# Kernel optimization log

Hardware: AMD Instinct MI355X
Metric: run time of the kernel (lower is better)

The kernel has to match this reference:

```python
import jax, jax.numpy as jnp
import numpy as np

N_SAMPLES = 32768


def fft_shift(a, shift):
    n = a.shape[-1]
    shift_samples = shift * (n / 3.0)  # trailing dim of shift is 1 -> broadcasts over coeffs
    pad = [(0, 0)] * (a.ndim - 1) + [(0, 2 * n)]
    spec = jnp.fft.rfft(jnp.pad(a, pad), axis=-1, norm='ortho')
    n_coeffs = spec.shape[-1]
    phase = jnp.arange(n_coeffs) * (2j * jnp.pi / n_coeffs)
    spec = spec * jnp.exp(-phase * shift_samples)
    out = jnp.fft.irfft(spec, n=3 * n, axis=-1, norm='ortho')
    return out[..., :n]


def interp_linear(x, out_size):
    # matches torch F.interpolate(mode='linear', align_corners=False)
    in_size = x.shape[-1]
    scale = in_size / out_size
    coords = (jnp.arange(out_size, dtype=x.dtype) + 0.5) * scale - 0.5
    coords = jnp.clip(coords, 0.0, in_size - 1)
    i0 = jnp.floor(coords).astype(jnp.int32)
    i1 = jnp.minimum(i0 + 1, in_size - 1)
    w = coords - i0.astype(x.dtype)
    return x[..., i0] * (1.0 - w) + x[..., i1] * w


def instrument(t, shift, energy, properties):
    batch, n_events, time_len = t.shape
    t = fft_shift(t, shift)  # (b,e,T)
    _, _, cp, n_frames = energy.shape
    frame_shifts = jnp.linspace(0.0, 1.0, n_frames)
    # (b,e,1,T) shifted per-frame -> (b,e,F,T)
    exp_t = fft_shift(t[:, :, None, :], frame_shifts[None, None, :, None])
    exp_t = exp_t[:, :, None, :, :]  # (b,e,1,F,T)
    # triu mask with offset 2: mask[i,j]=1 iff j >= i+2
    mask = (jnp.arange(time_len)[None, :] >= (jnp.arange(n_frames)[:, None] + 2)).astype(t.dtype)
    mask = fft_shift(mask[None, None], shift[:, :, None, :])  # (b,e,F,T)
    mass = properties[..., :1, None]      # (b,e,cp,1,1)
    friction = properties[..., 1:, None]  # (b,e,cp,1,1)
    x = energy[..., None] * jnp.exp(-friction / (2.0 * mass) * exp_t)  # (b,e,cp,F,T)
    x = x * mask[:, :, None, :, :]
    return jnp.sum(x, axis=-2)  # (b,e,cp,T)


def reference(time, shifts, energy, shape, properties, w_pos, b_pos, w_layers, b_layers):
    batch, n_events, cp, n_frames = energy.shape
    channels, enc = w_pos.shape
    # positional filterbank -> embed -> (1,1,channels,N)
    freqs = jnp.linspace(1e-05, 0.5, enc)
    tt = jnp.linspace(0.0, float(N_SAMPLES), N_SAMPLES)
    p = jnp.sin(tt[:, None] * freqs[None, :] * jnp.pi)  # (N, enc)
    pos = (p @ w_pos.T + b_pos).T[None, None]  # (1,1,channels,N)
    # envelopes
    env = instrument(time, shifts, energy, properties)  # (b,e,cp,T)
    env = jax.nn.relu(interp_linear(env, N_SAMPLES))    # (b,e,cp,N)
    # shape network (residual layers use only l2: x + l2(relu(x)))
    s = jnp.swapaxes(shape, -1, -2)  # (b,e,F,channels)
    for i in range(w_layers.shape[0]):
        s = s + jax.nn.relu(s) @ w_layers[i].T + b_layers[i]
    s = jax.nn.relu(s)
    s = jnp.swapaxes(s, -1, -2)           # (b,e,channels,F)
    s = interp_linear(s, N_SAMPLES)       # (b,e,channels,N)
    x = pos * s * env                      # cp == channels
    return jnp.sum(x, axis=2)              # (b,e,N)


def setup_inputs():
    key = jax.random.key(0)
    ks = jax.random.split(key, 9)
    B, E, CP, F_, T, CH, ENC, L = 2, 8, 32, 64, 2048, 32, 256, 4
    return {
        'time': jax.random.uniform(ks[0], (B, E, T), dtype=jnp.float32),
        'shifts': jax.random.uniform(ks[1], (B, E, 1), dtype=jnp.float32),
        'energy': jax.random.uniform(ks[2], (B, E, CP, F_), dtype=jnp.float32),
        'shape': jax.random.normal(ks[3], (B, E, CH, F_), dtype=jnp.float32),
        'properties': jax.random.uniform(ks[4], (B, E, CP, 2), dtype=jnp.float32) + 0.5,
        'w_pos': jax.random.normal(ks[5], (CH, ENC), dtype=jnp.float32) * 0.06,
        'b_pos': jax.random.normal(ks[6], (CH,), dtype=jnp.float32) * 0.02,
        'w_layers': jax.random.normal(ks[7], (L, CH, CH), dtype=jnp.float32) * 0.15,
        'b_layers': jax.random.normal(ks[8], (L, CH), dtype=jnp.float32) * 0.02,
    }
```

## Files before the change

### kernel.cpp

```cpp
#include <hip/hip_runtime.h>
#include <math.h>

#define TL 2048
#define PI_D 3.14159265358979323846

typedef __attribute__((ext_vector_type(8))) short short8v;
typedef __attribute__((ext_vector_type(4))) float float4v;

#define REPLEN 392
#define REPB (REPLEN * 2)
#define OFF_B 8192

__device__ __forceinline__ unsigned short bf16_rne(float f) {
  unsigned u = __float_as_uint(f);
  return (unsigned short)((u + 0x7FFFu + ((u >> 16) & 1u)) >> 16);
}

__device__ __forceinline__ float tap_val(int idx, double beta, double wv) {
  int d = idx - 2047;
  double x = PI_D * (double)d / 6144.0 - beta;
  if (fabs(x) < 1e-9) return 1.0f;
  double c = wv * (cos(x) / sin(x));
  if (d & 1) c = -c;
  return (float)c;
}

__global__ __launch_bounds__(256) void build_shift_k(const float* __restrict__ shifts,
                                                     const float* __restrict__ time_in,
                                                     float* __restrict__ kerC,
                                                     unsigned short* __restrict__ BFrep,
                                                     unsigned short* __restrict__ tsh_b) {
  __shared__ __align__(16) unsigned char sm1[17408];
  __shared__ float wsum[4];
  int b = blockIdx.x;
  int tid = threadIdx.x;
  if (b < 80) {
    float* kf = (float*)sm1;
    double s;
    if (b < 64) s = (double)b * (1.0 / 63.0) * (2048.0 / 3.0);
    else        s = (double)shifts[b - 64] * (2048.0 / 3.0);
    double beta = PI_D * s / 3073.0;
    double y = 3072.0 * s / 3073.0;
    double r = y - rint(y);
    double wv = -sin(2.0 * PI_D * r) / 6144.0;
    for (int idx = tid; idx < 4104; idx += 256)
      kf[idx] = (idx < 4095) ? tap_val(idx, beta, wv) : 0.0f;
    __syncthreads();
    if (b < 64) {
      for (int c = tid; c < 4096; c += 256) {
        int sr = c >> 9;
        int m = c & 511;
        int A = 4095 - 8 * m + sr;
        unsigned short out[8];
#pragma unroll
        for (int rr = 0; rr < 8; ++rr) out[rr] = bf16_rne(kf[A - rr]);
        *(short8v*)(BFrep + ((size_t)(b * 8 + sr)) * 4104 + 8 * m) = *(short8v*)out;
      }
    } else {
      float s0 = 0.f;
      int base = tid * 16;
#pragma unroll
      for (int i = 0; i < 16; ++i) s0 += kf[base + i];
      int lane = tid & 63;
      float v = s0;
#pragma unroll
      for (int d = 1; d < 64; d <<= 1) {
        float o = __shfl_up(v, (unsigned)d, 64);
        if (lane >= d) v += o;
      }
      if (lane == 63) wsum[tid >> 6] = v;
      __syncthreads();
      float woff = 0.f;
      for (int k = 0; k < (tid >> 6); ++k) woff += wsum[k];
      float run = v + woff - s0;
      float* crow = kerC + (b - 64) * 4096;
#pragma unroll
      for (int i = 0; i < 16; ++i) {
        crow[base + i] = run;
        run += kf[base + i];
      }
    }
  } else {
    int pb = b - 80;
    int p = pb >> 3, tile = pb & 7;
    float* a = (float*)sm1;
    float* kw = (float*)(sm1 + 8192);
    int t0 = tile * 256;
    double s = (double)shifts[p] * (2048.0 / 3.0);
    double beta = PI_D * s / 3073.0;
    double y = 3072.0 * s / 3073.0;
    double r = y - rint(y);
    double wv = -sin(2.0 * PI_D * r) / 6144.0;
    for (int i = tid; i < 2048; i += 256) a[i] = time_in[p * 2048 + i];
    for (int i = tid; i < 2303; i += 256) kw[i] = tap_val(t0 + i, beta, wv);
    __syncthreads();
    float acc = 0.f;
    int base = tid + 2047;
#pragma unroll 8
    for (int u = 0; u < 2048; ++u) acc = fmaf(a[u], kw[base - u], acc);
    tsh_b[p * 2048 + t0 + tid] = bf16_rne(acc);
  }
}

__global__ __launch_bounds__(256, 4) void fused_k(const unsigned short* __restrict__ tsh_b,
                                                  const unsigned short* __restrict__ BFrep,
                                                  float* __restrict__ expT,
                                                  const float* __restrict__ w_pos,
                                                  const float* __restrict__ b_pos,
                                                  float* __restrict__ pos,
                                                  const float* __restrict__ shape,
                                                  const float* __restrict__ w_layers,
                                                  const float* __restrict__ b_layers,
                                                  float* __restrict__ s64) {
  __shared__ __align__(16) unsigned char smem[21248];
  int bx = blockIdx.x;
  int tid = threadIdx.x;
  if (bx < 1024) {
    int j = bx >> 4;
    int tB = (bx & 15) << 7;
    int l = tid & 63, w = tid >> 6;
    int p16 = l & 15, g = l >> 4;
    int srep = l & 7, hb = (l >> 3) & 1;
    int h = w >> 1, kp = w & 1;
    int kc0 = kp << 2;

    float4v acc[4];
#pragma unroll
    for (int i = 0; i < 4; ++i) acc[i] = (float4v){0.f, 0.f, 0.f, 0.f};
    int bB2 = OFF_B + srep * REPB + 256 - (hb << 4) + (g << 4) - (h << 7);
    const unsigned short* grow = BFrep + (size_t)j * 8 * 4104;

    for (int ph = 0; ph < 8; ++ph) {
      int ub = ph << 8;
      int Q8 = 1912 - tB + ub;
      __syncthreads();
#pragma unroll
      for (int it = 0; it < 2; ++it) {
        int c = tid + (it << 8);
        int pp = c >> 5, m = c & 31;
        short8v v = *(const short8v*)(tsh_b + pp * 2048 + ub + (m << 3));
        int dst = ((pp << 9) + (m << 4)) ^ ((pp & 7) << 4);
        *(short8v*)(smem + dst) = v;
      }
      for (int c = tid; c < 384; c += 256) {
        int sr = c / 48;
        int m = c - sr * 48;
        short8v v = *(const short8v*)(grow + sr * 4104 + 8 + Q8 + (m << 3));
        *(short8v*)(smem + OFF_B + sr * REPB + (m << 4)) = v;
      }
      __syncthreads();
      int fb = bB2 + (kc0 << 6);
      short8v W0 = *(const short8v*)(smem + fb);
      short8v W1 = *(const short8v*)(smem + fb - 32);
      short8v W2 = *(const short8v*)(smem + fb - 64);
      short8v W3 = *(const short8v*)(smem + fb - 96);
#pragma unroll
      for (int qq = 0; qq < 4; ++qq) {
        int kc = kc0 + qq;
        if (qq > 0) {
          short8v t2 = W0, t3 = W1;
          W0 = *(const short8v*)(smem + fb + (qq << 6));
          W1 = *(const short8v*)(smem + fb + (qq << 6) - 32);
          W2 = t2;
          W3 = t3;
        }
        int ao = ((p16 << 9) + (kc << 6) + (g << 4)) ^ ((p16 & 7) << 4);
        short8v a = *(const short8v*)(smem + ao);
        acc[0] = __builtin_amdgcn_mfma_f32_16x16x32_bf16(a, W0, acc[0], 0, 0, 0);
        acc[1] = __builtin_amdgcn_mfma_f32_16x16x32_bf16(a, W1, acc[1], 0, 0, 0);
        acc[2] = __builtin_amdgcn_mfma_f32_16x16x32_bf16(a, W2, acc[2], 0, 0, 0);
        acc[3] = __builtin_amdgcn_mfma_f32_16x16x32_bf16(a, W3, acc[3], 0, 0, 0);
      }
    }
    __syncthreads();
    if (kp == 1) {
#pragma unroll
      for (int ct = 0; ct < 4; ++ct)
        *(float4v*)(smem + ((((h << 2) + ct) << 6) + l) * 16) = acc[ct];
    }
    __syncthreads();
    if (kp == 0) {
#pragma unroll
      for (int ct = 0; ct < 4; ++ct) {
        float4v o = *(const float4v*)(smem + ((((h << 2) + ct) << 6) + l) * 16);
#pragma unroll
        for (int rr = 0; rr < 4; ++rr) acc[ct][rr] += o[rr];
      }
      int tbase = tB + (h << 6) + p16;
#pragma unroll
      for (int ct = 0; ct < 4; ++ct) {
#pragma unroll
        for (int rr = 0; rr < 4; ++rr) {
          int prow = (g << 2) + rr;
          expT[(size_t)(prow * 64 + j) * TL + tbase + (ct << 4)] = acc[ct][rr];
        }
      }
    }
  } else if (bx < 1536) {
    int l = tid & 63, w = tid >> 6;
    int p16 = l & 15, g = l >> 4;
    int T0 = (bx - 1024) * 64 + w * 16;

    float ttv = (float)(T0 + p16) * (32768.0f / 32767.0f);
    float4v acc0 = {0.f, 0.f, 0.f, 0.f};
    float4v acc1 = {0.f, 0.f, 0.f, 0.f};
#pragma unroll
    for (int kc = 0; kc < 8; ++kc) {
      short8v bh0, bl0, bh1, bl1;
#pragma unroll
      for (int ct = 0; ct < 2; ++ct) {
        const float* wrow = w_pos + (ct * 16 + p16) * 256 + kc * 32 + g * 8;
        float4v w0 = *(const float4v*)(wrow);
        float4v w1 = *(const float4v*)(wrow + 4);
        short8v hv, lv;
#pragma unroll
        for (int i = 0; i < 8; ++i) {
          float vv = (i < 4) ? w0[i] : w1[i - 4];
          unsigned short hbit = bf16_rne(vv);
          float hf = __uint_as_float(((unsigned)hbit) << 16);
          hv[i] = (short)hbit;
          lv[i] = (short)bf16_rne(vv - hf);
        }
        if (ct == 0) { bh0 = hv; bl0 = lv; }
        else         { bh1 = hv; bl1 = lv; }
      }
      short8v ahi, alo;
#pragma unroll
      for (int i = 0; i < 8; ++i) {
        int f = kc * 32 + g * 8 + i;
        float fr = 1e-5f + (float)f * ((0.5f - 1e-5f) / 255.0f);
        float rev = ttv * (0.5f * fr);
        float sv = __builtin_amdgcn_sinf(__builtin_amdgcn_fractf(rev));
        unsigned short hbit = bf16_rne(sv);
        float hf = __uint_as_float(((unsigned)hbit) << 16);
        ahi[i] = (short)hbit;
        alo[i] = (short)bf16_rne(sv - hf);
      }
      acc0 = __builtin_amdgcn_mfma_f32_16x16x32_bf16(ahi, bh0, acc0, 0, 0, 0);
      acc1 = __builtin_amdgcn_mfma_f32_16x16x32_bf16(ahi, bh1, acc1, 0, 0, 0);
      acc0 = __builtin_amdgcn_mfma_f32_16x16x32_bf16(ahi, bl0, acc0, 0, 0, 0);
      acc1 = __builtin_amdgcn_mfma_f32_16x16x32_bf16(ahi, bl1, acc1, 0, 0, 0);
      acc0 = __builtin_amdgcn_mfma_f32_16x16x32_bf16(alo, bh0, acc0, 0, 0, 0);
      acc1 = __builtin_amdgcn_mfma_f32_16x16x32_bf16(alo, bh1, acc1, 0, 0, 0);
    }
    float bp0 = b_pos[p16], bp1 = b_pos[16 + p16];
    float4v o0, o1;
#pragma unroll
    for (int rr = 0; rr < 4; ++rr) {
      o0[rr] = acc0[rr] + bp0;
      o1[rr] = acc1[rr] + bp1;
    }
    int Tr = T0 + g * 4;
    *(float4v*)(pos + (size_t)p16 * 32768 + Tr) = o0;
    *(float4v*)(pos + (size_t)(16 + p16) * 32768 + Tr) = o1;
  } else {
    float(*sA)[33] = (float(*)[33])(smem);
    float(*sB)[33] = (float(*)[33])(smem + 8448);
    float(*W)[33] = (float(*)[33])(smem + 16896);
    float* bb = (float*)(smem + 21120);
    int p = bx - 1536;
    for (int idx = tid; idx < 2048; idx += 256) {
      int c = idx >> 6, f = idx & 63;
      sA[f][c] = shape[p * 2048 + idx];
    }
    int c = tid & 31, fg = tid >> 5;
    for (int ll = 0; ll < 4; ++ll) {
      for (int idx = tid; idx < 1024; idx += 256) W[idx >> 5][idx & 31] = w_layers[ll * 1024 + idx];
      if (tid < 32) bb[tid] = b_layers[ll * 32 + tid];
      __syncthreads();
      float(*cur)[33] = (ll & 1) ? sB : sA;
      float(*nxt)[33] = (ll & 1) ? sA : sB;
#pragma unroll
      for (int i = 0; i < 8; ++i) {
        int f = fg * 8 + i;
        float acc = cur[f][c] + bb[c];
#pragma unroll
        for (int k = 0; k < 32; ++k) acc = fmaf(fmaxf(cur[f][k], 0.f), W[c][k], acc);
        nxt[f][c] = acc;
      }
      __syncthreads();
    }
    for (int idx = tid; idx < 2048; idx += 256) {
      int cc = idx >> 6, f = idx & 63;
      s64[p * 2048 + idx] = fmaxf(sA[f][cc], 0.f);
    }
  }
}

__global__ __launch_bounds__(256) void env2_k(const float* __restrict__ energy,
                                              const float* __restrict__ props,
                                              const float* __restrict__ expT,
                                              const float* __restrict__ kerC,
                                              float* __restrict__ env) {
  int p = blockIdx.x >> 5, tile = blockIdx.x & 31;
  int tl = threadIdx.x & 63;
  int cg = threadIdx.x >> 6;
  int tC = tile * 64;
  int t = tC + tl;
  __shared__ float E[32][64];
  __shared__ float K[32];
  __shared__ float kcl[2112];
  for (int i = threadIdx.x; i < 2048; i += 256) E[i >> 6][i & 63] = energy[p * 2048 + i];
  const float* crow = kerC + p * 4096;
  for (int i = threadIdx.x; i < 2110; i += 256) kcl[i] = crow[tC + i];
  if (threadIdx.x < 32) {
    float mass = props[(p * 32 + threadIdx.x) * 2];
    float fric = props[(p * 32 + threadIdx.x) * 2 + 1];
    K[threadIdx.x] = fric / (2.0f * mass);
  }
  __syncthreads();
  float acc[8];
  float kk[8];
#pragma unroll
  for (int i = 0; i < 8; ++i) acc[i] = 0.f;
#pragma unroll
  for (int i = 0; i < 8; ++i) kk[i] = K[cg * 8 + i];
  float Ct = kcl[tl];
  const float* xrow = expT + (size_t)p * 64 * TL + t;
  for (int jj = 0; jj < 64; ++jj) {
    float x = xrow[jj * TL];
    float mv = kcl[tl + 2046 - jj] - Ct;
#pragma unroll
    for (int cc = 0; cc < 8; ++cc)
      acc[cc] = fmaf(E[cg * 8 + cc][jj] * mv, __expf(-kk[cc] * x), acc[cc]);
  }
#pragma unroll
  for (int cc = 0; cc < 8; ++cc)
    env[(size_t)(p * 32 + cg * 8 + cc) * TL + t] = acc[cc];
}

__global__ __launch_bounds__(256) void final_k(const float* __restrict__ pos,
                                               const float* __restrict__ s64,
                                               const float* __restrict__ env,
                                               float* __restrict__ out) {
  int gid = blockIdx.x * 256 + threadIdx.x;
  int p = gid >> 15, T = gid & 32767;
  float ft = (float)T + 0.5f;
  float ce = fminf(fmaxf(ft * 0.0625f - 0.5f, 0.f), 2047.f);
  int ie = (int)ce;
  int ie1 = min(ie + 1, 2047);
  float we = ce - (float)ie;
  float cs = fminf(fmaxf(ft * (1.0f / 512.0f) - 0.5f, 0.f), 63.f);
  int is0 = (int)cs;
  int is1 = min(is0 + 1, 63);
  float ws = cs - (float)is0;
  const float* erow = env + (size_t)p * 32 * TL;
  const float* srow = s64 + p * 32 * 64;
  float acc = 0.f;
  for (int c = 0; c < 32; ++c) {
    float pv = pos[(size_t)c * 32768 + T];
    float ev = fmaxf(erow[c * TL + ie] * (1.f - we) + erow[c * TL + ie1] * we, 0.f);
    float sv = srow[c * 64 + is0] * (1.f - ws) + srow[c * 64 + is1] * ws;
    acc += pv * sv * ev;
  }
  out[gid] = acc;
}

extern "C" void kernel_launch(void* const* d_in, const int* in_sizes, int n_in,
                              void* d_out, int out_size, void* d_ws, size_t ws_size,
                              hipStream_t stream) {
  const float* time_in  = (const float*)d_in[0];
  const float* shifts   = (const float*)d_in[1];
  const float* energy   = (const float*)d_in[2];
  const float* shape    = (const float*)d_in[3];
  const float* props    = (const float*)d_in[4];
  const float* w_pos    = (const float*)d_in[5];
  const float* b_pos    = (const float*)d_in[6];
  const float* w_layers = (const float*)d_in[7];
  const float* b_layers = (const float*)d_in[8];

  float* ws = (float*)d_ws;
  float* kerC = ws;
  unsigned short* BFrep = (unsigned short*)(ws + 65536);
  unsigned short* tsh_b = (unsigned short*)(ws + 1116160);
  float* expT = ws + 1132544;
  float* env  = ws + 3229696;
  float* pos  = ws + 4278272;
  float* s64  = ws + 5326848;
  float* out  = (float*)d_out;

  hipLaunchKernelGGL(build_shift_k, dim3(208), dim3(256), 0, stream,
                     shifts, time_in, kerC, BFrep, tsh_b);
  hipLaunchKernelGGL(fused_k, dim3(1552), dim3(256), 0, stream, tsh_b, BFrep, expT,
                     w_pos, b_pos, pos, shape, w_layers, b_layers, s64);
  hipLaunchKernelGGL(env2_k, dim3(512), dim3(256), 0, stream, energy, props, expT, kerC, env);
  hipLaunchKernelGGL(final_k, dim3(2048), dim3(256), 0, stream, pos, s64, env, out);
}
```

Baseline: 102.9 us.

## Fuse envelope and final kernels, precompute split-bf16 weights, split shift conv

Merges the envelope and final interpolation kernels into one kernel. Each block recomputes a haloed env tile in shared memory, so the env buffer no longer makes a global round trip and one launch is removed. The w_pos hi/lo bf16 split moves into the first kernel as a precomputed buffer, and the pos MFMA drops the alo term, going from 6 to 4 MFMAs per step at some precision cost. The time-shift convolution is split across two half-ranges per block with a shared-memory reduction to double the block count. The fused_k block order and the pos/s64 block ranges are also rearranged.

New measurement: 122.8 us. 19.3% more time.

```diff
diff --git a/kernel.cpp b/kernel.cpp
--- a/kernel.cpp
+++ b/kernel.cpp
@@ -7,8 +7,7 @@
 typedef __attribute__((ext_vector_type(8))) short short8v;
 typedef __attribute__((ext_vector_type(4))) float float4v;
 
-#define REPLEN 392
-#define REPB (REPLEN * 2)
+#define REPB 784
 #define OFF_B 8192
 
 __device__ __forceinline__ unsigned short bf16_rne(float f) {
@@ -27,9 +26,11 @@
 
 __global__ __launch_bounds__(256) void build_shift_k(const float* __restrict__ shifts,
                                                      const float* __restrict__ time_in,
+                                                     const float* __restrict__ w_pos,
                                                      float* __restrict__ kerC,
                                                      unsigned short* __restrict__ BFrep,
-                                                     unsigned short* __restrict__ tsh_b) {
+                                                     unsigned short* __restrict__ tsh_b,
+                                                     unsigned short* __restrict__ Whl) {
   __shared__ __align__(16) unsigned char sm1[17408];
   __shared__ float wsum[4];
   int b = blockIdx.x;
@@ -80,32 +81,62 @@
         run += kf[base + i];
       }
     }
-  } else {
-    int pb = b - 80;
-    int p = pb >> 3, tile = pb & 7;
+  } else if (b < 336) {
+    int idx = b - 80;
+    int p = idx >> 4, tile = idx & 15;
+    int t0 = tile * 128;
     float* a = (float*)sm1;
     float* kw = (float*)(sm1 + 8192);
-    int t0 = tile * 256;
+    float* partial = (float*)(sm1 + 16896);
     double s = (double)shifts[p] * (2048.0 / 3.0);
     double beta = PI_D * s / 3073.0;
     double y = 3072.0 * s / 3073.0;
     double r = y - rint(y);
     double wv = -sin(2.0 * PI_D * r) / 6144.0;
     for (int i = tid; i < 2048; i += 256) a[i] = time_in[p * 2048 + i];
-    for (int i = tid; i < 2303; i += 256) kw[i] = tap_val(t0 + i, beta, wv);
-    __syncthreads();
+    for (int i = tid; i < 2175; i += 256) kw[i] = tap_val(t0 + i, beta, wv);
+    __syncthreads();
+    int tl = tid & 127, uh = tid >> 7;
+    int base = tl + 2047 - (uh << 10);
+    int u0 = uh << 10;
     float acc = 0.f;
-    int base = tid + 2047;
 #pragma unroll 8
-    for (int u = 0; u < 2048; ++u) acc = fmaf(a[u], kw[base - u], acc);
-    tsh_b[p * 2048 + t0 + tid] = bf16_rne(acc);
+    for (int u2 = 0; u2 < 1024; ++u2) acc = fmaf(a[u0 + u2], kw[base - u2], acc);
+    __syncthreads();
+    if (uh == 1) partial[tl] = acc;
+    __syncthreads();
+    if (uh == 0) {
+      acc += partial[tl];
+      tsh_b[p * 2048 + t0 + tl] = bf16_rne(acc);
+    }
+  } else {
+    int c0 = (b - 336) * 1024 + tid * 4;
+#pragma unroll
+    for (int k2 = 0; k2 < 4; ++k2) {
+      int c = c0 + k2;
+      int sel = c & 1, g = (c >> 1) & 3, p16v = (c >> 3) & 15;
+      int kc = (c >> 7) & 7, ct = c >> 10;
+      const float* wrow = w_pos + (ct * 16 + p16v) * 256 + kc * 32 + g * 8;
+      short8v ov;
+#pragma unroll
+      for (int i = 0; i < 8; ++i) {
+        float vv = wrow[i];
+        unsigned short hb = bf16_rne(vv);
+        if (sel == 0) ov[i] = (short)hb;
+        else {
+          float hf = __uint_as_float(((unsigned)hb) << 16);
+          ov[i] = (short)bf16_rne(vv - hf);
+        }
+      }
+      *(short8v*)(Whl + (size_t)c * 8) = ov;
+    }
   }
 }
 
 __global__ __launch_bounds__(256, 4) void fused_k(const unsigned short* __restrict__ tsh_b,
                                                   const unsigned short* __restrict__ BFrep,
                                                   float* __restrict__ expT,
-                                                  const float* __restrict__ w_pos,
+                                                  const unsigned short* __restrict__ Whl,
                                                   const float* __restrict__ b_pos,
                                                   float* __restrict__ pos,
                                                   const float* __restrict__ shape,
@@ -116,8 +147,8 @@
   int bx = blockIdx.x;
   int tid = threadIdx.x;
   if (bx < 1024) {
-    int j = bx >> 4;
-    int tB = (bx & 15) << 7;
+    int j = bx & 63;
+    int tB = (bx >> 6) << 7;
     int l = tid & 63, w = tid >> 6;
     int p16 = l & 15, g = l >> 4;
     int srep = l & 7, hb = (l >> 3) & 1;
@@ -196,69 +227,12 @@
         }
       }
     }
-  } else if (bx < 1536) {
-    int l = tid & 63, w = tid >> 6;
-    int p16 = l & 15, g = l >> 4;
-    int T0 = (bx - 1024) * 64 + w * 16;
-
-    float ttv = (float)(T0 + p16) * (32768.0f / 32767.0f);
-    float4v acc0 = {0.f, 0.f, 0.f, 0.f};
-    float4v acc1 = {0.f, 0.f, 0.f, 0.f};
-#pragma unroll
-    for (int kc = 0; kc < 8; ++kc) {
-      short8v bh0, bl0, bh1, bl1;
-#pragma unroll
-      for (int ct = 0; ct < 2; ++ct) {
-        const float* wrow = w_pos + (ct * 16 + p16) * 256 + kc * 32 + g * 8;
-        float4v w0 = *(const float4v*)(wrow);
-        float4v w1 = *(const float4v*)(wrow + 4);
-        short8v hv, lv;
-#pragma unroll
-        for (int i = 0; i < 8; ++i) {
-          float vv = (i < 4) ? w0[i] : w1[i - 4];
-          unsigned short hbit = bf16_rne(vv);
-          float hf = __uint_as_float(((unsigned)hbit) << 16);
-          hv[i] = (short)hbit;
-          lv[i] = (short)bf16_rne(vv - hf);
-        }
-        if (ct == 0) { bh0 = hv; bl0 = lv; }
-        else         { bh1 = hv; bl1 = lv; }
-      }
-      short8v ahi, alo;
-#pragma unroll
-      for (int i = 0; i < 8; ++i) {
-        int f = kc * 32 + g * 8 + i;
-        float fr = 1e-5f + (float)f * ((0.5f - 1e-5f) / 255.0f);
-        float rev = ttv * (0.5f * fr);
-        float sv = __builtin_amdgcn_sinf(__builtin_amdgcn_fractf(rev));
-        unsigned short hbit = bf16_rne(sv);
-        float hf = __uint_as_float(((unsigned)hbit) << 16);
-        ahi[i] = (short)hbit;
-        alo[i] = (short)bf16_rne(sv - hf);
-      }
-      acc0 = __builtin_amdgcn_mfma_f32_16x16x32_bf16(ahi, bh0, acc0, 0, 0, 0);
-      acc1 = __builtin_amdgcn_mfma_f32_16x16x32_bf16(ahi, bh1, acc1, 0, 0, 0);
-      acc0 = __builtin_amdgcn_mfma_f32_16x16x32_bf16(ahi, bl0, acc0, 0, 0, 0);
-      acc1 = __builtin_amdgcn_mfma_f32_16x16x32_bf16(ahi, bl1, acc1, 0, 0, 0);
-      acc0 = __builtin_amdgcn_mfma_f32_16x16x32_bf16(alo, bh0, acc0, 0, 0, 0);
-      acc1 = __builtin_amdgcn_mfma_f32_16x16x32_bf16(alo, bh1, acc1, 0, 0, 0);
-    }
-    float bp0 = b_pos[p16], bp1 = b_pos[16 + p16];
-    float4v o0, o1;
-#pragma unroll
-    for (int rr = 0; rr < 4; ++rr) {
-      o0[rr] = acc0[rr] + bp0;
-      o1[rr] = acc1[rr] + bp1;
-    }
-    int Tr = T0 + g * 4;
-    *(float4v*)(pos + (size_t)p16 * 32768 + Tr) = o0;
-    *(float4v*)(pos + (size_t)(16 + p16) * 32768 + Tr) = o1;
-  } else {
+  } else if (bx < 1040) {
     float(*sA)[33] = (float(*)[33])(smem);
     float(*sB)[33] = (float(*)[33])(smem + 8448);
     float(*W)[33] = (float(*)[33])(smem + 16896);
     float* bb = (float*)(smem + 21120);
-    int p = bx - 1536;
+    int p = bx - 1024;
     for (int idx = tid; idx < 2048; idx += 256) {
       int c = idx >> 6, f = idx & 63;
       sA[f][c] = shape[p * 2048 + idx];
@@ -284,76 +258,123 @@
       int cc = idx >> 6, f = idx & 63;
       s64[p * 2048 + idx] = fmaxf(sA[f][cc], 0.f);
     }
-  }
-}
-
-__global__ __launch_bounds__(256) void env2_k(const float* __restrict__ energy,
-                                              const float* __restrict__ props,
-                                              const float* __restrict__ expT,
-                                              const float* __restrict__ kerC,
-                                              float* __restrict__ env) {
-  int p = blockIdx.x >> 5, tile = blockIdx.x & 31;
-  int tl = threadIdx.x & 63;
-  int cg = threadIdx.x >> 6;
-  int tC = tile * 64;
-  int t = tC + tl;
+  } else {
+    int l = tid & 63, w = tid >> 6;
+    int p16 = l & 15, g = l >> 4;
+    int T0 = (bx - 1040) * 64 + w * 16;
+
+    float ttv = (float)(T0 + p16) * (32768.0f / 32767.0f);
+    float4v acc0 = {0.f, 0.f, 0.f, 0.f};
+    float4v acc1 = {0.f, 0.f, 0.f, 0.f};
+    const short8v* Wt = (const short8v*)Whl;
+    int fbase = (p16 << 3) + (g << 1);
+#pragma unroll
+    for (int kc = 0; kc < 8; ++kc) {
+      short8v bh0 = Wt[(kc << 7) + fbase];
+      short8v bl0 = Wt[(kc << 7) + fbase + 1];
+      short8v bh1 = Wt[1024 + (kc << 7) + fbase];
+      short8v bl1 = Wt[1024 + (kc << 7) + fbase + 1];
+      short8v a;
+#pragma unroll
+      for (int i = 0; i < 8; ++i) {
+        int f = kc * 32 + g * 8 + i;
+        float fr = 1e-5f + (float)f * ((0.5f - 1e-5f) / 255.0f);
+        float rev = ttv * (0.5f * fr);
+        float sv = __builtin_amdgcn_sinf(__builtin_amdgcn_fractf(rev));
+        a[i] = (short)bf16_rne(sv);
+      }
+      acc0 = __builtin_amdgcn_mfma_f32_16x16x32_bf16(a, bh0, acc0, 0, 0, 0);
+      acc1 = __builtin_amdgcn_mfma_f32_16x16x32_bf16(a, bh1, acc1, 0, 0, 0);
+      acc0 = __builtin_amdgcn_mfma_f32_16x16x32_bf16(a, bl0, acc0, 0, 0, 0);
+      acc1 = __builtin_amdgcn_mfma_f32_16x16x32_bf16(a, bl1, acc1, 0, 0, 0);
+    }
+    float bp0 = b_pos[p16], bp1 = b_pos[16 + p16];
+    float4v o0, o1;
+#pragma unroll
+    for (int rr = 0; rr < 4; ++rr) {
+      o0[rr] = acc0[rr] + bp0;
+      o1[rr] = acc1[rr] + bp1;
+    }
+    int Tr = T0 + g * 4;
+    *(float4v*)(pos + (size_t)p16 * 32768 + Tr) = o0;
+    *(float4v*)(pos + (size_t)(16 + p16) * 32768 + Tr) = o1;
+  }
+}
+
+__global__ __launch_bounds__(256) void envfinal_k(const float* __restrict__ energy,
+                                                  const float* __restrict__ props,
+                                                  const float* __restrict__ expT,
+                                                  const float* __restrict__ kerC,
+                                                  const float* __restrict__ pos,
+                                                  const float* __restrict__ s64,
+                                                  float* __restrict__ out) {
   __shared__ float E[32][64];
   __shared__ float K[32];
   __shared__ float kcl[2112];
-  for (int i = threadIdx.x; i < 2048; i += 256) E[i >> 6][i & 63] = energy[p * 2048 + i];
+  __shared__ float env_s[32][72];
+  int p = blockIdx.x >> 5, tile = blockIdx.x & 31;
+  int tid = threadIdx.x;
+  int tC = tile * 64;
+  int tCm1 = tC - 1;
+  for (int i = tid; i < 2048; i += 256) E[i >> 6][i & 63] = energy[p * 2048 + i];
   const float* crow = kerC + p * 4096;
-  for (int i = threadIdx.x; i < 2110; i += 256) kcl[i] = crow[tC + i];
-  if (threadIdx.x < 32) {
-    float mass = props[(p * 32 + threadIdx.x) * 2];
-    float fric = props[(p * 32 + threadIdx.x) * 2 + 1];
-    K[threadIdx.x] = fric / (2.0f * mass);
+  for (int i = tid; i < 2112; i += 256) {
+    int gidx = tCm1 + i;
+    kcl[i] = (gidx >= 0 && gidx < 4096) ? crow[gidx] : 0.f;
+  }
+  if (tid < 32) {
+    float mass = props[(p * 32 + tid) * 2];
+    float fric = props[(p * 32 + tid) * 2 + 1];
+    K[tid] = fric / (2.0f * mass);
   }
   __syncthreads();
-  float acc[8];
+  int tl = tid & 63, cg = tid >> 6;
   float kk[8];
 #pragma unroll
-  for (int i = 0; i < 8; ++i) acc[i] = 0.f;
-#pragma unroll
   for (int i = 0; i < 8; ++i) kk[i] = K[cg * 8 + i];
-  float Ct = kcl[tl];
-  const float* xrow = expT + (size_t)p * 64 * TL + t;
-  for (int jj = 0; jj < 64; ++jj) {
-    float x = xrow[jj * TL];
-    float mv = kcl[tl + 2046 - jj] - Ct;
-#pragma unroll
-    for (int cc = 0; cc < 8; ++cc)
-      acc[cc] = fmaf(E[cg * 8 + cc][jj] * mv, __expf(-kk[cc] * x), acc[cc]);
-  }
-#pragma unroll
-  for (int cc = 0; cc < 8; ++cc)
-    env[(size_t)(p * 32 + cg * 8 + cc) * TL + t] = acc[cc];
-}
-
-__global__ __launch_bounds__(256) void final_k(const float* __restrict__ pos,
-                                               const float* __restrict__ s64,
-                                               const float* __restrict__ env,
-                                               float* __restrict__ out) {
-  int gid = blockIdx.x * 256 + threadIdx.x;
-  int p = gid >> 15, T = gid & 32767;
-  float ft = (float)T + 0.5f;
-  float ce = fminf(fmaxf(ft * 0.0625f - 0.5f, 0.f), 2047.f);
-  int ie = (int)ce;
-  int ie1 = min(ie + 1, 2047);
-  float we = ce - (float)ie;
-  float cs = fminf(fmaxf(ft * (1.0f / 512.0f) - 0.5f, 0.f), 63.f);
-  int is0 = (int)cs;
-  int is1 = min(is0 + 1, 63);
-  float ws = cs - (float)is0;
-  const float* erow = env + (size_t)p * 32 * TL;
-  const float* srow = s64 + p * 32 * 64;
-  float acc = 0.f;
-  for (int c = 0; c < 32; ++c) {
-    float pv = pos[(size_t)c * 32768 + T];
-    float ev = fmaxf(erow[c * TL + ie] * (1.f - we) + erow[c * TL + ie1] * we, 0.f);
-    float sv = srow[c * 64 + is0] * (1.f - ws) + srow[c * 64 + is1] * ws;
-    acc += pv * sv * ev;
-  }
-  out[gid] = acc;
+  for (int tt = tl; tt < 66; tt += 64) {
+    int t = tCm1 + tt;
+    int tc = t < 0 ? 0 : (t > 2047 ? 2047 : t);
+    float Ct = kcl[tt];
+    const float* xrow = expT + (size_t)p * 64 * TL + tc;
+    float acc[8];
+#pragma unroll
+    for (int i = 0; i < 8; ++i) acc[i] = 0.f;
+    for (int jj = 0; jj < 64; ++jj) {
+      float x = xrow[jj * TL];
+      float mv = kcl[tt + 2047 - jj] - Ct;
+#pragma unroll
+      for (int cc = 0; cc < 8; ++cc)
+        acc[cc] = fmaf(E[cg * 8 + cc][jj] * mv, __expf(-kk[cc] * x), acc[cc]);
+    }
+#pragma unroll
+    for (int cc = 0; cc < 8; ++cc) env_s[cg * 8 + cc][tt] = acc[cc];
+  }
+  __syncthreads();
+  int T0 = tile * 1024;
+  const float* srow = s64 + p * 2048;
+#pragma unroll
+  for (int q = 0; q < 4; ++q) {
+    int T = T0 + q * 256 + tid;
+    float ft = (float)T + 0.5f;
+    float ce = fminf(fmaxf(ft * 0.0625f - 0.5f, 0.f), 2047.f);
+    int ie = (int)ce;
+    int ie1 = min(ie + 1, 2047);
+    float we = ce - (float)ie;
+    int iel = ie - tCm1, iel1 = ie1 - tCm1;
+    float cs = fminf(fmaxf(ft * (1.0f / 512.0f) - 0.5f, 0.f), 63.f);
+    int is0 = (int)cs;
+    int is1 = min(is0 + 1, 63);
+    float ws = cs - (float)is0;
+    float acc = 0.f;
+    for (int c = 0; c < 32; ++c) {
+      float pv = pos[(size_t)c * 32768 + T];
+      float ev = fmaxf(env_s[c][iel] * (1.f - we) + env_s[c][iel1] * we, 0.f);
+      float sv = srow[c * 64 + is0] * (1.f - ws) + srow[c * 64 + is1] * ws;
+      acc += pv * sv * ev;
+    }
+    out[(size_t)p * 32768 + T] = acc;
+  }
 }
 
 extern "C" void kernel_launch(void* const* d_in, const int* in_sizes, int n_in,
@@ -374,15 +395,15 @@
   unsigned short* BFrep = (unsigned short*)(ws + 65536);
   unsigned short* tsh_b = (unsigned short*)(ws + 1116160);
   float* expT = ws + 1132544;
-  float* env  = ws + 3229696;
-  float* pos  = ws + 4278272;
-  float* s64  = ws + 5326848;
+  float* pos  = ws + 3229696;
+  float* s64  = ws + 4278272;
+  unsigned short* Whl = (unsigned short*)(ws + 4311040);
   float* out  = (float*)d_out;
 
-  hipLaunchKernelGGL(build_shift_k, dim3(208), dim3(256), 0, stream,
-                     shifts, time_in, kerC, BFrep, tsh_b);
+  hipLaunchKernelGGL(build_shift_k, dim3(340), dim3(256), 0, stream,
+                     shifts, time_in, w_pos, kerC, BFrep, tsh_b, Whl);
   hipLaunchKernelGGL(fused_k, dim3(1552), dim3(256), 0, stream, tsh_b, BFrep, expT,
-                     w_pos, b_pos, pos, shape, w_layers, b_layers, s64);
-  hipLaunchKernelGGL(env2_k, dim3(512), dim3(256), 0, stream, energy, props, expT, kerC, env);
-  hipLaunchKernelGGL(final_k, dim3(2048), dim3(256), 0, stream, pos, s64, env, out);
-}
+                     Whl, b_pos, pos, shape, w_layers, b_layers, s64);
+  hipLaunchKernelGGL(envfinal_k, dim3(512), dim3(256), 0, stream,
+                     energy, props, expT, kerC, pos, s64, out);
+}
```
